# Optimization experiments

Hardware: AMD Instinct MI355X
Metric: run time of the kernel (lower is better)

Reference implementation:

```python
import jax, jax.numpy as jnp
import numpy as np

N = 8192   # num_nodes
K = 64     # neighbors per node
BN_EPS = 1e-3  # keras BatchNormalization default epsilon


def setup_inputs() -> dict:
    key = jax.random.key(0)
    ks = jax.random.split(key, 8)
    input_data = jax.random.normal(ks[0], (1, N), dtype=jnp.float32)
    adj = jax.random.randint(ks[1], (N, K), 0, N, dtype=jnp.int64)
    edge_weights = jax.random.uniform(ks[2], (N, K), dtype=jnp.float32)
    # update_fn = BatchNorm -> Dropout(inference: identity) -> Dense(N, gelu) on [1, 2N]
    W = jax.random.normal(ks[3], (2 * N, N), dtype=jnp.float32) * 0.02
    b = jnp.zeros((N,), dtype=jnp.float32)
    bn_gamma = jnp.ones((2 * N,), dtype=jnp.float32)
    bn_beta = jnp.zeros((2 * N,), dtype=jnp.float32)
    bn_mean = jnp.zeros((2 * N,), dtype=jnp.float32)
    bn_var = jnp.ones((2 * N,), dtype=jnp.float32)
    return {"input_data": input_data, "adj": adj, "edge_weights": edge_weights,
            "W": W, "b": b, "bn_gamma": bn_gamma, "bn_beta": bn_beta,
            "bn_mean": bn_mean, "bn_var": bn_var}


def reference(input_data, adj, edge_weights, W, b, bn_gamma, bn_beta, bn_mean, bn_var):
    x = input_data[0]                    # [N] per-node expression
    ngh_sum = jnp.sum(x[adj], axis=1)    # gather [N,K] then sum over neighbors -> [N]
    agg = x + ngh_sum                    # 'sum' aggregation adds self
    h = jnp.concatenate([x, agg])[None, :]  # 'concat' combination -> [1, 2N]
    # BatchNorm (inference mode, moving stats)
    h = (h - bn_mean) * jax.lax.rsqrt(bn_var + BN_EPS) * bn_gamma + bn_beta
    # Dropout is identity at inference; Dense with exact (erf) gelu as in tf.nn.gelu
    out = jax.nn.gelu(h @ W + b, approximate=False)  # [1, N]
    return out
```

## Files before the change

### kernel.cpp

```cpp
#include <hip/hip_runtime.h>
#include <math.h>

#define BN_EPS 1e-3f

#define GB_ROWS 64
#define GB_COLS 1024

typedef float floatx4 __attribute__((ext_vector_type(4)));

__global__ void agg_bn_kernel(const float* __restrict__ x,
                              const int* __restrict__ adj,
                              const float* __restrict__ bn_gamma,
                              const float* __restrict__ bn_beta,
                              const float* __restrict__ bn_mean,
                              const float* __restrict__ bn_var,
                              float* __restrict__ h_bn,
                              int N, int K)
{
    int gid  = blockIdx.x * blockDim.x + threadIdx.x;
    int node = gid >> 6;
    int lane = gid & 63;
    if (node >= N) return;

    float s = 0.0f;
    for (int k = lane; k < K; k += 64) {
        int nb = adj[(size_t)node * K + k];
        s += x[nb];
    }
#pragma unroll
    for (int off = 32; off > 0; off >>= 1)
        s += __shfl_down(s, off, 64);

    if (lane == 0) {
        float xi  = x[node];
        float agg = xi + s;
        {
            float sc = rsqrtf(bn_var[node] + BN_EPS) * bn_gamma[node];
            h_bn[node] = (xi - bn_mean[node]) * sc + bn_beta[node];
        }
        {
            int j = N + node;
            float sc = rsqrtf(bn_var[j] + BN_EPS) * bn_gamma[j];
            h_bn[j] = (agg - bn_mean[j]) * sc + bn_beta[j];
        }
    }
}

__global__ __launch_bounds__(256, 8)
void gemv_partial_kernel(const float* __restrict__ h,
                         const float* __restrict__ W,
                         float* __restrict__ part,
                         int N)
{
    __shared__ float hs[GB_ROWS];
    int row0 = blockIdx.y * GB_ROWS;
    if (threadIdx.x < GB_ROWS)
        hs[threadIdx.x] = h[row0 + threadIdx.x];
    __syncthreads();

    int col = blockIdx.x * GB_COLS + threadIdx.x * 4;
    const float* Wp = W + (size_t)row0 * N + col;

    float ax = 0.0f, ay = 0.0f, az = 0.0f, aw = 0.0f;
#pragma unroll 8
    for (int r = 0; r < GB_ROWS; ++r) {
        floatx4 w = __builtin_nontemporal_load(
            reinterpret_cast<const floatx4*>(Wp));
        float hv = hs[r];
        ax = fmaf(hv, w.x, ax);
        ay = fmaf(hv, w.y, ay);
        az = fmaf(hv, w.z, az);
        aw = fmaf(hv, w.w, aw);
        Wp += N;
    }
    floatx4 o = { ax, ay, az, aw };
    *reinterpret_cast<floatx4*>(part + (size_t)blockIdx.y * N + col) = o;
}

__global__ __launch_bounds__(256)
void reduce_bias_gelu_kernel(const float* __restrict__ part,
                             const float* __restrict__ b,
                             float* __restrict__ out,
                             int N, int RY)
{
    __shared__ float sm[4][64];
    int lane = threadIdx.x & 63;
    int wv   = threadIdx.x >> 6;
    int col  = blockIdx.x * 64 + lane;

    float s = 0.0f;
    for (int ry = wv; ry < RY; ry += 4)
        s += part[(size_t)ry * N + col];
    sm[wv][lane] = s;
    __syncthreads();

    if (threadIdx.x < 64) {
        float v = sm[0][lane] + sm[1][lane] + sm[2][lane] + sm[3][lane] + b[col];
        out[col] = 0.5f * v * (1.0f + erff(v * 0.70710678118654752f));
    }
}

extern "C" void kernel_launch(void* const* d_in, const int* in_sizes, int n_in,
                              void* d_out, int out_size, void* d_ws, size_t ws_size,
                              hipStream_t stream)
{
    const float* x   = (const float*)d_in[0];
    const int*   adj = (const int*)d_in[1];
    const float* W   = (const float*)d_in[3];
    const float* b   = (const float*)d_in[4];
    const float* g   = (const float*)d_in[5];
    const float* be  = (const float*)d_in[6];
    const float* mn  = (const float*)d_in[7];
    const float* vr  = (const float*)d_in[8];
    float* out = (float*)d_out;

    int N = in_sizes[0];
    int K = in_sizes[1] / N;
    int RY = (2 * N) / GB_ROWS;

    float* part = (float*)d_ws;
    float* h_bn = part + (size_t)RY * N;

    {
        long long total_threads = (long long)N * 64;
        int threads = 256;
        int blocks = (int)((total_threads + threads - 1) / threads);
        agg_bn_kernel<<<blocks, threads, 0, stream>>>(x, adj, g, be, mn, vr, h_bn, N, K);
    }
    {
        dim3 grid(N / GB_COLS, RY);
        gemv_partial_kernel<<<grid, 256, 0, stream>>>(h_bn, W, part, N);
    }
    reduce_bias_gelu_kernel<<<N / 64, 256, 0, stream>>>(part, b, out, N, RY);
}
```

Before: 707.7 us.

## Fuse aggregation, GEMV and reduction into one cooperative persistent kernel

Replaces the three launches (aggregation+BN, partial GEMV, reduce+bias+GELU) with a single cooperative kernel of 1024 persistent blocks that uses grid-wide syncs between phases. The aim is to remove launch gaps and tail effects between kernels. In exchange it adds two grid barriers and a grid-stride loop over GEMV chunks with extra __syncthreads per chunk. It also drops the nontemporal loads on W, which may change cache behaviour for the 512MB weight stream.

```diff
diff --git a/kernel.cpp b/kernel.cpp
--- a/kernel.cpp
+++ b/kernel.cpp
@@ -1,102 +1,104 @@
 #include <hip/hip_runtime.h>
+#include <hip/hip_cooperative_groups.h>
 #include <math.h>
 
+namespace cg = cooperative_groups;
+
 #define BN_EPS 1e-3f
+
+#define NBLK 1024
+#define NTHR 256
 
 #define GB_ROWS 64
 #define GB_COLS 1024
 
-typedef float floatx4 __attribute__((ext_vector_type(4)));
+__global__ __launch_bounds__(NTHR, 4)
+void fused_gcn_kernel(const float* __restrict__ x,
+                      const int* __restrict__ adj,
+                      const float* __restrict__ bn_gamma,
+                      const float* __restrict__ bn_beta,
+                      const float* __restrict__ bn_mean,
+                      const float* __restrict__ bn_var,
+                      const float* __restrict__ W,
+                      const float* __restrict__ b,
+                      float* __restrict__ part,
+                      float* __restrict__ h_bn,
+                      float* __restrict__ out,
+                      int N, int K)
+{
+    cg::grid_group grid = cg::this_grid();
+    __shared__ float hs[GB_ROWS];
+    __shared__ float sm[4][64];
 
-__global__ void agg_bn_kernel(const float* __restrict__ x,
-                              const int* __restrict__ adj,
-                              const float* __restrict__ bn_gamma,
-                              const float* __restrict__ bn_beta,
-                              const float* __restrict__ bn_mean,
-                              const float* __restrict__ bn_var,
-                              float* __restrict__ h_bn,
-                              int N, int K)
-{
-    int gid  = blockIdx.x * blockDim.x + threadIdx.x;
-    int node = gid >> 6;
-    int lane = gid & 63;
-    if (node >= N) return;
+    const int tid  = threadIdx.x;
+    const int lane = tid & 63;
+    const int wv   = tid >> 6;
 
-    float s = 0.0f;
-    for (int k = lane; k < K; k += 64) {
-        int nb = adj[(size_t)node * K + k];
-        s += x[nb];
-    }
+    const int nodes_per_blk = (N + NBLK - 1) / NBLK;
+    for (int ni = 0; ni < nodes_per_blk; ni += 4) {
+        int node = blockIdx.x * nodes_per_blk + ni + wv;
+        if (node < N) {
+            float s = 0.0f;
+            for (int k = lane; k < K; k += 64)
+                s += x[adj[(size_t)node * K + k]];
 #pragma unroll
-    for (int off = 32; off > 0; off >>= 1)
-        s += __shfl_down(s, off, 64);
-
-    if (lane == 0) {
-        float xi  = x[node];
-        float agg = xi + s;
-        {
-            float sc = rsqrtf(bn_var[node] + BN_EPS) * bn_gamma[node];
-            h_bn[node] = (xi - bn_mean[node]) * sc + bn_beta[node];
-        }
-        {
-            int j = N + node;
-            float sc = rsqrtf(bn_var[j] + BN_EPS) * bn_gamma[j];
-            h_bn[j] = (agg - bn_mean[j]) * sc + bn_beta[j];
+            for (int off = 32; off > 0; off >>= 1)
+                s += __shfl_down(s, off, 64);
+            if (lane == 0) {
+                float xi  = x[node];
+                float agg = xi + s;
+                float sc0 = rsqrtf(bn_var[node] + BN_EPS) * bn_gamma[node];
+                h_bn[node] = (xi - bn_mean[node]) * sc0 + bn_beta[node];
+                int j = N + node;
+                float sc1 = rsqrtf(bn_var[j] + BN_EPS) * bn_gamma[j];
+                h_bn[j] = (agg - bn_mean[j]) * sc1 + bn_beta[j];
+            }
         }
     }
-}
 
-__global__ __launch_bounds__(256, 8)
-void gemv_partial_kernel(const float* __restrict__ h,
-                         const float* __restrict__ W,
-                         float* __restrict__ part,
-                         int N)
-{
-    __shared__ float hs[GB_ROWS];
-    int row0 = blockIdx.y * GB_ROWS;
-    if (threadIdx.x < GB_ROWS)
-        hs[threadIdx.x] = h[row0 + threadIdx.x];
-    __syncthreads();
+    grid.sync();
 
-    int col = blockIdx.x * GB_COLS + threadIdx.x * 4;
-    const float* Wp = W + (size_t)row0 * N + col;
+    const int ncol_blk = N / GB_COLS;
+    const int nchunks  = (2 * N / GB_ROWS) * ncol_blk;
+    for (int c = blockIdx.x; c < nchunks; c += NBLK) {
+        int bx   = c & (ncol_blk - 1);
+        int by   = c / ncol_blk;
+        int row0 = by * GB_ROWS;
 
-    float ax = 0.0f, ay = 0.0f, az = 0.0f, aw = 0.0f;
+        if (tid < GB_ROWS) hs[tid] = h_bn[row0 + tid];
+        __syncthreads();
+
+        int col = bx * GB_COLS + tid * 4;
+        const float* Wp = W + (size_t)row0 * N + col;
+        float ax = 0.0f, ay = 0.0f, az = 0.0f, aw = 0.0f;
 #pragma unroll 8
-    for (int r = 0; r < GB_ROWS; ++r) {
-        floatx4 w = __builtin_nontemporal_load(
-            reinterpret_cast<const floatx4*>(Wp));
-        float hv = hs[r];
-        ax = fmaf(hv, w.x, ax);
-        ay = fmaf(hv, w.y, ay);
-        az = fmaf(hv, w.z, az);
-        aw = fmaf(hv, w.w, aw);
-        Wp += N;
+        for (int r = 0; r < GB_ROWS; ++r) {
+            float4 w = *(const float4*)Wp;
+            float hv = hs[r];
+            ax = fmaf(hv, w.x, ax);
+            ay = fmaf(hv, w.y, ay);
+            az = fmaf(hv, w.z, az);
+            aw = fmaf(hv, w.w, aw);
+            Wp += N;
+        }
+        *(float4*)(part + (size_t)by * N + col) = make_float4(ax, ay, az, aw);
+        __syncthreads();
     }
-    floatx4 o = { ax, ay, az, aw };
-    *reinterpret_cast<floatx4*>(part + (size_t)blockIdx.y * N + col) = o;
-}
 
-__global__ __launch_bounds__(256)
-void reduce_bias_gelu_kernel(const float* __restrict__ part,
-                             const float* __restrict__ b,
-                             float* __restrict__ out,
-                             int N, int RY)
-{
-    __shared__ float sm[4][64];
-    int lane = threadIdx.x & 63;
-    int wv   = threadIdx.x >> 6;
-    int col  = blockIdx.x * 64 + lane;
+    grid.sync();
 
-    float s = 0.0f;
-    for (int ry = wv; ry < RY; ry += 4)
-        s += part[(size_t)ry * N + col];
-    sm[wv][lane] = s;
-    __syncthreads();
-
-    if (threadIdx.x < 64) {
-        float v = sm[0][lane] + sm[1][lane] + sm[2][lane] + sm[3][lane] + b[col];
-        out[col] = 0.5f * v * (1.0f + erff(v * 0.70710678118654752f));
+    if (blockIdx.x < N / 64) {
+        const int RY  = 2 * N / GB_ROWS;
+        int col = blockIdx.x * 64 + lane;
+        float s = 0.0f;
+        for (int ry = wv; ry < RY; ry += 4)
+            s += part[(size_t)ry * N + col];
+        sm[wv][lane] = s;
+        __syncthreads();
+        if (tid < 64) {
+            float v = sm[0][lane] + sm[1][lane] + sm[2][lane] + sm[3][lane] + b[col];
+            out[col] = 0.5f * v * (1.0f + erff(v * 0.70710678118654752f));
+        }
     }
 }
 
@@ -121,15 +123,11 @@
     float* part = (float*)d_ws;
     float* h_bn = part + (size_t)RY * N;
 
-    {
-        long long total_threads = (long long)N * 64;
-        int threads = 256;
-        int blocks = (int)((total_threads + threads - 1) / threads);
-        agg_bn_kernel<<<blocks, threads, 0, stream>>>(x, adj, g, be, mn, vr, h_bn, N, K);
-    }
-    {
-        dim3 grid(N / GB_COLS, RY);
-        gemv_partial_kernel<<<grid, 256, 0, stream>>>(h_bn, W, part, N);
-    }
-    reduce_bias_gelu_kernel<<<N / 64, 256, 0, stream>>>(part, b, out, N, RY);
+    void* args[] = {
+        (void*)&x, (void*)&adj, (void*)&g, (void*)&be, (void*)&mn, (void*)&vr,
+        (void*)&W, (void*)&b, (void*)&part, (void*)&h_bn, (void*)&out,
+        (void*)&N, (void*)&K
+    };
+    hipLaunchCooperativeKernel((void*)fused_gcn_kernel,
+                               dim3(NBLK), dim3(NTHR), args, 0, stream);
 }
```

After: 904.1 us. +27.7%, slower.

## Restructure GEMV into full-row slabs with double-buffered multi-stream loads

Applied to the files above, without the earlier changes.

The GEMV now gives each block 16 full rows of W instead of a 64x1024 tile. Each thread keeps 8 float4 streams across the row and double-buffers the loads of consecutive rows, so far more memory requests are in flight per thread. This produces four times as many partial rows, so a new two-stage reduction (reduce8, then the bias+gelu reduce) combines them, at the cost of extra partial-buffer traffic and workspace. The nontemporal load hint is also dropped.

```diff
diff --git a/kernel.cpp b/kernel.cpp
--- a/kernel.cpp
+++ b/kernel.cpp
@@ -3,10 +3,8 @@
 
 #define BN_EPS 1e-3f
 
-#define GB_ROWS 64
-#define GB_COLS 1024
-
-typedef float floatx4 __attribute__((ext_vector_type(4)));
+#define RPB 16
+#define NSTREAM 8
 
 __global__ void agg_bn_kernel(const float* __restrict__ x,
                               const int* __restrict__ adj,
@@ -23,10 +21,8 @@
     if (node >= N) return;
 
     float s = 0.0f;
-    for (int k = lane; k < K; k += 64) {
-        int nb = adj[(size_t)node * K + k];
-        s += x[nb];
-    }
+    for (int k = lane; k < K; k += 64)
+        s += x[adj[(size_t)node * K + k]];
 #pragma unroll
     for (int off = 32; off > 0; off >>= 1)
         s += __shfl_down(s, off, 64);
@@ -34,54 +30,86 @@
     if (lane == 0) {
         float xi  = x[node];
         float agg = xi + s;
-        {
-            float sc = rsqrtf(bn_var[node] + BN_EPS) * bn_gamma[node];
-            h_bn[node] = (xi - bn_mean[node]) * sc + bn_beta[node];
-        }
-        {
-            int j = N + node;
-            float sc = rsqrtf(bn_var[j] + BN_EPS) * bn_gamma[j];
-            h_bn[j] = (agg - bn_mean[j]) * sc + bn_beta[j];
-        }
+        float sc0 = rsqrtf(bn_var[node] + BN_EPS) * bn_gamma[node];
+        h_bn[node] = (xi - bn_mean[node]) * sc0 + bn_beta[node];
+        int j = N + node;
+        float sc1 = rsqrtf(bn_var[j] + BN_EPS) * bn_gamma[j];
+        h_bn[j] = (agg - bn_mean[j]) * sc1 + bn_beta[j];
     }
 }
 
-__global__ __launch_bounds__(256, 8)
-void gemv_partial_kernel(const float* __restrict__ h,
-                         const float* __restrict__ W,
-                         float* __restrict__ part,
-                         int N)
+#define LOADROW(dst, r) {                                                  \
+    const float4* p_ = Wrow + (size_t)(r) * Nq;                            \
+    _Pragma("unroll")                                                      \
+    for (int s_ = 0; s_ < NSTREAM; ++s_) dst[s_] = p_[s_ * 256]; }
+
+#define FMAROW(src, r) {                                                   \
+    float hv_ = hs[(r)];                                                   \
+    _Pragma("unroll")                                                      \
+    for (int s_ = 0; s_ < NSTREAM; ++s_) {                                 \
+        acc[s_].x = fmaf(hv_, src[s_].x, acc[s_].x);                       \
+        acc[s_].y = fmaf(hv_, src[s_].y, acc[s_].y);                       \
+        acc[s_].z = fmaf(hv_, src[s_].z, acc[s_].z);                       \
+        acc[s_].w = fmaf(hv_, src[s_].w, acc[s_].w); } }
+
+__global__ __launch_bounds__(256, 4)
+void gemv_slab_kernel(const float* __restrict__ h,
+                      const float* __restrict__ W,
+                      float* __restrict__ part,
+                      int N)
 {
-    __shared__ float hs[GB_ROWS];
-    int row0 = blockIdx.y * GB_ROWS;
-    if (threadIdx.x < GB_ROWS)
-        hs[threadIdx.x] = h[row0 + threadIdx.x];
+    __shared__ float hs[RPB];
+    int row0 = blockIdx.x * RPB;
+    if (threadIdx.x < RPB) hs[threadIdx.x] = h[row0 + threadIdx.x];
     __syncthreads();
 
-    int col = blockIdx.x * GB_COLS + threadIdx.x * 4;
-    const float* Wp = W + (size_t)row0 * N + col;
+    const int tcol = threadIdx.x * 4;
+    const int Nq = N >> 2;
+    const float4* Wrow = (const float4*)(W + (size_t)row0 * N + tcol);
 
-    float ax = 0.0f, ay = 0.0f, az = 0.0f, aw = 0.0f;
-#pragma unroll 8
-    for (int r = 0; r < GB_ROWS; ++r) {
-        floatx4 w = __builtin_nontemporal_load(
-            reinterpret_cast<const floatx4*>(Wp));
-        float hv = hs[r];
-        ax = fmaf(hv, w.x, ax);
-        ay = fmaf(hv, w.y, ay);
-        az = fmaf(hv, w.z, az);
-        aw = fmaf(hv, w.w, aw);
-        Wp += N;
+    float4 acc[NSTREAM];
+#pragma unroll
+    for (int s = 0; s < NSTREAM; ++s) acc[s] = make_float4(0.f, 0.f, 0.f, 0.f);
+
+    float4 wA[NSTREAM], wB[NSTREAM];
+    LOADROW(wA, 0);
+#pragma unroll
+    for (int r = 0; r < RPB; r += 2) {
+        LOADROW(wB, r + 1);
+        FMAROW(wA, r);
+        if (r + 2 < RPB) LOADROW(wA, r + 2);
+        FMAROW(wB, r + 1);
     }
-    floatx4 o = { ax, ay, az, aw };
-    *reinterpret_cast<floatx4*>(part + (size_t)blockIdx.y * N + col) = o;
+
+    float* pp = part + (size_t)blockIdx.x * N + tcol;
+#pragma unroll
+    for (int s = 0; s < NSTREAM; ++s)
+        *(float4*)(pp + s * (N >> 3)) = acc[s];
 }
 
 __global__ __launch_bounds__(256)
-void reduce_bias_gelu_kernel(const float* __restrict__ part,
+void reduce8_kernel(const float* __restrict__ part,
+                    float* __restrict__ part2,
+                    int N)
+{
+    int g   = blockIdx.x >> 3;
+    int seg = blockIdx.x & 7;
+    int col = seg * (N >> 3) + threadIdx.x * 4;
+    const float* p = part + (size_t)(g * 8) * N + col;
+    float4 s = make_float4(0.f, 0.f, 0.f, 0.f);
+#pragma unroll
+    for (int i = 0; i < 8; ++i) {
+        float4 v = *(const float4*)(p + (size_t)i * N);
+        s.x += v.x; s.y += v.y; s.z += v.z; s.w += v.w;
+    }
+    *(float4*)(part2 + (size_t)g * N + col) = s;
+}
+
+__global__ __launch_bounds__(256)
+void reduce_bias_gelu_kernel(const float* __restrict__ part2,
                              const float* __restrict__ b,
                              float* __restrict__ out,
-                             int N, int RY)
+                             int N, int G2)
 {
     __shared__ float sm[4][64];
     int lane = threadIdx.x & 63;
@@ -89,8 +117,8 @@
     int col  = blockIdx.x * 64 + lane;
 
     float s = 0.0f;
-    for (int ry = wv; ry < RY; ry += 4)
-        s += part[(size_t)ry * N + col];
+    for (int g = wv; g < G2; g += 4)
+        s += part2[(size_t)g * N + col];
     sm[wv][lane] = s;
     __syncthreads();
 
@@ -114,22 +142,21 @@
     const float* vr  = (const float*)d_in[8];
     float* out = (float*)d_out;
 
-    int N = in_sizes[0];
-    int K = in_sizes[1] / N;
-    int RY = (2 * N) / GB_ROWS;
+    int N  = in_sizes[0];
+    int K  = in_sizes[1] / N;
+    int PB = (2 * N) / RPB;
+    int G2 = PB / 8;
 
-    float* part = (float*)d_ws;
-    float* h_bn = part + (size_t)RY * N;
+    float* part  = (float*)d_ws;
+    float* part2 = part + (size_t)PB * N;
+    float* h_bn  = part2 + (size_t)G2 * N;
 
     {
         long long total_threads = (long long)N * 64;
-        int threads = 256;
-        int blocks = (int)((total_threads + threads - 1) / threads);
-        agg_bn_kernel<<<blocks, threads, 0, stream>>>(x, adj, g, be, mn, vr, h_bn, N, K);
+        int blocks = (int)((total_threads + 255) / 256);
+        agg_bn_kernel<<<blocks, 256, 0, stream>>>(x, adj, g, be, mn, vr, h_bn, N, K);
     }
-    {
-        dim3 grid(N / GB_COLS, RY);
-        gemv_partial_kernel<<<grid, 256, 0, stream>>>(h_bn, W, part, N);
-    }
-    reduce_bias_gelu_kernel<<<N / 64, 256, 0, stream>>>(part, b, out, N, RY);
+    gemv_slab_kernel<<<PB, 256, 0, stream>>>(h_bn, W, part, N);
+    reduce8_kernel<<<PB, 256, 0, stream>>>(part, part2, N);
+    reduce_bias_gelu_kernel<<<N / 64, 256, 0, stream>>>(part2, b, out, N, G2);
 }
```

Result: no change. 709.8 us (+0.3%).
